# Kernel optimization log

Measured on AMD Instinct MI355X. Metric: run time of the kernel, lower is better.

Reference implementation:

```python
import jax, jax.numpy as jnp
import numpy as np

C = 4        # num_case (3) + coreference (1)
H = 128      # self.hidden_size
D = 768      # bert hidden size
B, S = 2, 384


def setup_inputs() -> dict:
    key = jax.random.key(0)
    ks = jax.random.split(key, 9)
    sc = 0.02
    return {
        "sequence_output": jax.random.normal(ks[0], (B, S, D), jnp.float32),
        "base_score": jax.random.uniform(ks[1], (B, S, C, S), jnp.float32),
        "W_prd_w": jax.random.normal(ks[2], (D, C * H), jnp.float32) * sc,
        "W_prd_b": jnp.zeros((C * H,), jnp.float32),
        "U_arg_w": jax.random.normal(ks[3], (D, C * H), jnp.float32) * sc,
        "U_arg_b": jnp.zeros((C * H,), jnp.float32),
        "W_mid": jax.random.normal(ks[4], (H * (C + 2), H), jnp.float32) * sc,
        "b_mid": jnp.zeros((H,), jnp.float32),
        "w_out": jax.random.normal(ks[5], (H,), jnp.float32) * sc,
    }


def reference(sequence_output, base_score, W_prd_w, W_prd_b, U_arg_w, U_arg_b, W_mid, b_mid, w_out):
    b, s, _ = sequence_output.shape
    # projections (dropout = identity in eval)
    h_p = (sequence_output @ W_prd_w + W_prd_b).reshape(b, s, C, H)   # [B,S,C,H]
    h_a = (sequence_output @ U_arg_w + U_arg_b).reshape(b, s, C, H)   # [B,S,C,H]
    # weighted_sum over argument positions: base_score[b,prd,case,arg]
    ref = jnp.einsum("bach,bpca->bpch", h_a, base_score).reshape(b, s, C * H)  # [B,S,C*H]
    # mid_layer(tanh(cat[prd_rep, h_a, ref])) == sum of three block matmuls,
    # since tanh is elementwise on each concatenated block.
    W1, W2, W3 = W_mid[:H], W_mid[H:2 * H], W_mid[2 * H:]
    t_prd = jnp.einsum("bpch,hk->bpck", jnp.tanh(h_p), W1)   # [B,Sp,C,H]
    t_arg = jnp.einsum("bach,hk->back", jnp.tanh(h_a), W2)   # [B,Sa,C,H]
    t_ref = jnp.tanh(ref) @ W3                                # [B,Sp,H]
    h_mid = (t_prd[:, :, None, :, :] + t_arg[:, None, :, :, :]
             + t_ref[:, :, None, None, :] + b_mid)            # [B,Sp,Sa,C,H]
    out = jnp.tanh(h_mid) @ w_out                             # [B,Sp,Sa,C]
    return out.transpose(0, 1, 3, 2)                          # [B,Sp,C,Sa]
```

## Files before the change

### kernel.cpp

```cpp
#include <hip/hip_runtime.h>
#include <hip/hip_bf16.h>


#define C2 2.885390081777927f

typedef __attribute__((ext_vector_type(8))) __bf16 bf16x8;
typedef __attribute__((ext_vector_type(8))) unsigned short ushort8;
typedef __attribute__((ext_vector_type(4))) float float4v;

__device__ __forceinline__ unsigned short f2bf(float f) {
  unsigned int u = __float_as_uint(f);
  u += 0x7fffu + ((u >> 16) & 1u);
  return (unsigned short)(u >> 16);
}

__device__ __forceinline__ float fast_tanh(float x) {
  float e = __builtin_amdgcn_exp2f(C2 * x);
  return 1.0f - 2.0f * __builtin_amdgcn_rcpf(1.0f + e);
}

__device__ __forceinline__ void gemm_core(
    const float* __restrict__ Abase, int lda,
    const float* __restrict__ Bbase, int ldb, int K,
    unsigned short* Alds, unsigned short* Blds,
    int ar, int ac, int bk, int bn,
    int wm0, int wn0, int col16, int quad, float4v acc[2][2])
{
  const float* Ap = Abase + (size_t)ar * lda + ac;
  const float* Bp = Bbase + (size_t)bk * ldb + bn;
  float4 a0 = ((const float4*)Ap)[0], a1 = ((const float4*)Ap)[1];
  float4 b0 = ((const float4*)Bp)[0], b1 = ((const float4*)Bp)[1];

  for (int k0 = 0; k0 < K; k0 += 32) {
    __syncthreads();
    {
      ushort8 o;
      o[0] = f2bf(a0.x); o[1] = f2bf(a0.y); o[2] = f2bf(a0.z); o[3] = f2bf(a0.w);
      o[4] = f2bf(a1.x); o[5] = f2bf(a1.y); o[6] = f2bf(a1.z); o[7] = f2bf(a1.w);
      *(ushort8*)&Alds[ar * 40 + ac] = o;
      float vv[8] = {b0.x, b0.y, b0.z, b0.w, b1.x, b1.y, b1.z, b1.w};
#pragma unroll
      for (int j = 0; j < 8; ++j) Blds[(bn + j) * 40 + bk] = f2bf(vv[j]);
    }
    __syncthreads();
    if (k0 + 32 < K) {
      const float4* An = (const float4*)(Ap + k0 + 32);
      const float4* Bn = (const float4*)(Bp + (size_t)(k0 + 32) * ldb);
      a0 = An[0]; a1 = An[1]; b0 = Bn[0]; b1 = Bn[1];
    }
    bf16x8 afrag[2], bfrag[2];
#pragma unroll
    for (int i = 0; i < 2; ++i)
      afrag[i] = __builtin_bit_cast(bf16x8,
          *(const ushort8*)&Alds[(wm0 + i * 16 + col16) * 40 + quad * 8]);
#pragma unroll
    for (int j = 0; j < 2; ++j)
      bfrag[j] = __builtin_bit_cast(bf16x8,
          *(const ushort8*)&Blds[(wn0 + j * 16 + col16) * 40 + quad * 8]);
#pragma unroll
    for (int i = 0; i < 2; ++i)
#pragma unroll
      for (int j = 0; j < 2; ++j)
        acc[i][j] = __builtin_amdgcn_mfma_f32_16x16x32_bf16(
            afrag[i], bfrag[j], acc[i][j], 0, 0, 0);
  }
}

__global__ __launch_bounds__(256) void g1_dual(
    const float* __restrict__ seq, const float* __restrict__ Wp,
    const float* __restrict__ Ua, const float* __restrict__ Wpb,
    const float* __restrict__ Uab, float* __restrict__ tanh_out,
    float* __restrict__ h_a, float* __restrict__ tref_clear)
{
  const int z = blockIdx.z;
  if (z == 2) {
    int idx = ((blockIdx.y * 8 + blockIdx.x) * 256 + threadIdx.x) * 4;
    *(float4*)&tref_clear[idx] = float4{0.f, 0.f, 0.f, 0.f};
    return;
  }
  __shared__ unsigned short Alds[64 * 40];
  __shared__ unsigned short Blds[64 * 40];
  const int tid = threadIdx.x;
  const int bn0 = blockIdx.x * 64, bm0 = blockIdx.y * 64;
  const int wid = tid >> 6, lane = tid & 63;
  const int wm0 = (wid >> 1) * 32, wn0 = (wid & 1) * 32;
  const int col16 = lane & 15, quad = lane >> 4;
  const float* B = z ? Ua : Wp;
  const float* bias = z ? Uab : Wpb;

  float4v acc[2][2];
#pragma unroll
  for (int i = 0; i < 2; ++i)
#pragma unroll
    for (int j = 0; j < 2; ++j) acc[i][j] = (float4v)(0.f);

  gemm_core(seq + (size_t)bm0 * 768, 768, B + bn0, 512, 768,
            Alds, Blds, tid >> 2, (tid & 3) * 8, tid >> 3, (tid & 7) * 8,
            wm0, wn0, col16, quad, acc);

  float* tout = tanh_out + (size_t)z * 393216;
#pragma unroll
  for (int j = 0; j < 2; ++j) {
    const int gcol = bn0 + wn0 + j * 16 + col16;
    const float bv = bias[gcol];
#pragma unroll
    for (int i = 0; i < 2; ++i)
#pragma unroll
      for (int r = 0; r < 4; ++r) {
        const int grow = bm0 + wm0 + i * 16 + quad * 4 + r;
        const float x = acc[i][j][r] + bv;
        const size_t cidx = (size_t)grow * 512 + gcol;
        tout[cidx] = fast_tanh(x);
        if (z == 1) h_a[cidx] = x;
      }
  }
}

__global__ __launch_bounds__(256) void fused_mid(
    const float* __restrict__ base, const float* __restrict__ h_a,
    const float* __restrict__ tanh_h, const float* __restrict__ Wmid,
    float* __restrict__ tprd_s, unsigned short* __restrict__ targ_s,
    float* __restrict__ tref_s)
{
  __shared__ unsigned short Alds[64 * 40];
  __shared__ unsigned short Blds[64 * 40];
  __shared__ unsigned short TA[64 * 72];
  __shared__ unsigned short TB[128 * 72];

  const int tid = threadIdx.x;
  const int bid = blockIdx.x;
  const int wid = tid >> 6, lane = tid & 63;
  const int wm0 = (wid >> 1) * 32, wn0 = (wid & 1) * 32;
  const int col16 = lane & 15, quad = lane >> 4;
  const int ar = tid >> 2, ac = (tid & 3) * 8;
  const int bk = tid >> 3, bn = (tid & 7) * 8;

  float4v acc[2][2];
#pragma unroll
  for (int i = 0; i < 2; ++i)
#pragma unroll
    for (int j = 0; j < 2; ++j) acc[i][j] = (float4v)(0.f);

  if (bid < 96) {
    const int z = bid / 12, rem = bid % 12;
    const int b = z >> 2, c = z & 3;
    const int y = rem >> 1, x = rem & 1;
    const float* A = base + (size_t)b * 589824 + c * 384 + (size_t)(y * 64) * 1536;
    const float* Bm = h_a + (size_t)b * 196608 + c * 128 + x * 64;
    gemm_core(A, 1536, Bm, 512, 384, Alds, Blds, ar, ac, bk, bn,
              wm0, wn0, col16, quad, acc);

#pragma unroll
    for (int j = 0; j < 2; ++j)
#pragma unroll
      for (int i = 0; i < 2; ++i)
#pragma unroll
        for (int r = 0; r < 4; ++r)
          TA[(wm0 + i * 16 + quad * 4 + r) * 72 + wn0 + j * 16 + col16] =
              f2bf(fast_tanh(acc[i][j][r]));
    {
      const float* W3p = Wmid + 32768 + (size_t)(c * 128 + x * 64) * 128;
      const int kr = tid >> 2, nb = (tid & 3) * 32;
#pragma unroll
      for (int q = 0; q < 8; ++q) {
        float4 v = *(const float4*)(W3p + (size_t)kr * 128 + nb + q * 4);
        TB[(nb + q * 4 + 0) * 72 + kr] = f2bf(v.x);
        TB[(nb + q * 4 + 1) * 72 + kr] = f2bf(v.y);
        TB[(nb + q * 4 + 2) * 72 + kr] = f2bf(v.z);
        TB[(nb + q * 4 + 3) * 72 + kr] = f2bf(v.w);
      }
    }
    __syncthreads();

    const int mh = wid & 1, nh = wid >> 1;
    float4v acc2[2][4];
#pragma unroll
    for (int i = 0; i < 2; ++i)
#pragma unroll
      for (int j = 0; j < 4; ++j) acc2[i][j] = (float4v)(0.f);
#pragma unroll
    for (int ks = 0; ks < 2; ++ks) {
      bf16x8 af[2], bf[4];
#pragma unroll
      for (int i = 0; i < 2; ++i)
        af[i] = __builtin_bit_cast(bf16x8,
            *(const ushort8*)&TA[(mh * 32 + i * 16 + col16) * 72 + ks * 32 + quad * 8]);
#pragma unroll
      for (int j = 0; j < 4; ++j)
        bf[j] = __builtin_bit_cast(bf16x8,
            *(const ushort8*)&TB[(nh * 64 + j * 16 + col16) * 72 + ks * 32 + quad * 8]);
#pragma unroll
      for (int i = 0; i < 2; ++i)
#pragma unroll
        for (int j = 0; j < 4; ++j)
          acc2[i][j] = __builtin_amdgcn_mfma_f32_16x16x32_bf16(
              af[i], bf[j], acc2[i][j], 0, 0, 0);
    }
#pragma unroll
    for (int j = 0; j < 4; ++j) {
      const int gcol = nh * 64 + j * 16 + col16;
#pragma unroll
      for (int i = 0; i < 2; ++i)
#pragma unroll
        for (int r = 0; r < 4; ++r) {
          const int grow = b * 384 + y * 64 + mh * 32 + i * 16 + quad * 4 + r;
          atomicAdd(&tref_s[(size_t)grow * 128 + gcol], C2 * acc2[i][j][r]);
        }
    }
  } else {
    const int idx = bid - 96;
    const int x = idx & 1, y = (idx >> 1) % 48, z = idx / 96;
    const float* A = tanh_h + (size_t)z * 393216 + (size_t)(y * 64) * 128;
    const float* Bm = Wmid + z * 16384 + x * 64;
    gemm_core(A, 128, Bm, 128, 128, Alds, Blds, ar, ac, bk, bn,
              wm0, wn0, col16, quad, acc);
#pragma unroll
    for (int j = 0; j < 2; ++j) {
      const int gcol = x * 64 + wn0 + j * 16 + col16;
#pragma unroll
      for (int i = 0; i < 2; ++i)
#pragma unroll
        for (int r = 0; r < 4; ++r) {
          const int grow = y * 64 + wm0 + i * 16 + quad * 4 + r;
          const float v = C2 * acc[i][j][r];
          const size_t cidx = (size_t)grow * 128 + gcol;
          if (z == 0) tprd_s[cidx] = v;
          else        targ_s[cidx] = f2bf(v);
        }
    }
  }
}

__global__ __launch_bounds__(256) void phase2(
    const float* __restrict__ tprd, const unsigned short* __restrict__ targ,
    const float* __restrict__ tref, const float* __restrict__ bmid,
    const float* __restrict__ wout, float* __restrict__ out)
{
  __shared__ float Es[8 * 128];
  __shared__ float Ws[128];
  __shared__ float Red[128 * 9];

  const int tid = threadIdx.x;
  const int a = tid & 127, kh = tid >> 7;
  const int p0 = blockIdx.x * 8, a0 = blockIdx.y * 128;
  const int b = blockIdx.z >> 2, c = blockIdx.z & 3;

  const uint4* grow = (const uint4*)((const unsigned int*)targ +
      (size_t)((b * 384 + a0 + a) * 4 + c) * 64 + kh * 32);
  uint4 G[8];
#pragma unroll
  for (int i = 0; i < 8; ++i) G[i] = grow[i];

  if (tid < 128) Ws[tid] = -2.f * wout[tid];
#pragma unroll
  for (int it = 0; it < 4; ++it) {
    int idx = it * 256 + tid;
    int p = idx >> 7, k = idx & 127;
    int row = b * 384 + p0 + p;
    Es[idx] = __builtin_amdgcn_exp2f(
        tprd[(size_t)(row * 4 + c) * 128 + k] +
        tref[(size_t)row * 128 + k] + C2 * bmid[k]);
  }
  float sw = 0.f;
  for (int k4 = 0; k4 < 32; ++k4) {
    float4 w = ((const float4*)wout)[k4];
    sw += w.x + w.y + w.z + w.w;
  }
  __syncthreads();

  float acc[8];
#pragma unroll
  for (int p = 0; p < 8; ++p) acc[p] = 0.f;

  const int kb0 = kh * 64;
#pragma unroll
  for (int j = 0; j < 8; ++j) {
    const uint4 gq = G[j];
    const float eg0 = __builtin_amdgcn_exp2f(__uint_as_float(gq.x << 16));
    const float eg1 = __builtin_amdgcn_exp2f(__uint_as_float(gq.x & 0xffff0000u));
    const float eg2 = __builtin_amdgcn_exp2f(__uint_as_float(gq.y << 16));
    const float eg3 = __builtin_amdgcn_exp2f(__uint_as_float(gq.y & 0xffff0000u));
    const float eg4 = __builtin_amdgcn_exp2f(__uint_as_float(gq.z << 16));
    const float eg5 = __builtin_amdgcn_exp2f(__uint_as_float(gq.z & 0xffff0000u));
    const float eg6 = __builtin_amdgcn_exp2f(__uint_as_float(gq.w << 16));
    const float eg7 = __builtin_amdgcn_exp2f(__uint_as_float(gq.w & 0xffff0000u));
    const int kb = kb0 + j * 8;
    const float4 wqA = *(const float4*)&Ws[kb];
    const float4 wqB = *(const float4*)&Ws[kb + 4];
#pragma unroll
    for (int p = 0; p < 8; ++p) {
      const float4 efA = *(const float4*)&Es[p * 128 + kb];
      const float4 efB = *(const float4*)&Es[p * 128 + kb + 4];
      float d0 = fmaf(efA.x, eg0, 1.f);
      float d1 = fmaf(efA.y, eg1, 1.f);
      float d2 = fmaf(efA.z, eg2, 1.f);
      float d3 = fmaf(efA.w, eg3, 1.f);
      float d01 = d0 * d1, d23 = d2 * d3;
      float n01 = fmaf(wqA.y, d0, wqA.x * d1);
      float n23 = fmaf(wqA.w, d2, wqA.z * d3);
      float num = fmaf(n01, d23, n23 * d01);
      acc[p] = fmaf(num, __builtin_amdgcn_rcpf(d01 * d23), acc[p]);
      d0 = fmaf(efB.x, eg4, 1.f);
      d1 = fmaf(efB.y, eg5, 1.f);
      d2 = fmaf(efB.z, eg6, 1.f);
      d3 = fmaf(efB.w, eg7, 1.f);
      d01 = d0 * d1; d23 = d2 * d3;
      n01 = fmaf(wqB.y, d0, wqB.x * d1);
      n23 = fmaf(wqB.w, d2, wqB.z * d3);
      num = fmaf(n01, d23, n23 * d01);
      acc[p] = fmaf(num, __builtin_amdgcn_rcpf(d01 * d23), acc[p]);
    }
  }

  if (kh) {
#pragma unroll
    for (int p = 0; p < 8; ++p) Red[a * 9 + p] = acc[p];
  }
  __syncthreads();
  if (!kh) {
    const size_t ob = (size_t)((b * 384 + p0) * 4 + c) * 384 + a0 + a;
#pragma unroll
    for (int p = 0; p < 8; ++p)
      out[ob + (size_t)p * 1536] = sw + acc[p] + Red[a * 9 + p];
  }
}

extern "C" void kernel_launch(void* const* d_in, const int* in_sizes, int n_in,
                              void* d_out, int out_size, void* d_ws, size_t ws_size,
                              hipStream_t stream) {
  (void)in_sizes; (void)n_in; (void)out_size; (void)ws_size;
  const float* seq  = (const float*)d_in[0];
  const float* base = (const float*)d_in[1];
  const float* Wp   = (const float*)d_in[2];
  const float* Wpb  = (const float*)d_in[3];
  const float* Ua   = (const float*)d_in[4];
  const float* Uab  = (const float*)d_in[5];
  const float* Wmid = (const float*)d_in[6];
  const float* bmid = (const float*)d_in[7];
  const float* wout = (const float*)d_in[8];
  float* out = (float*)d_out;

  float* ws = (float*)d_ws;
  float* tanh_h = ws;
  float* h_a    = ws + 786432;
  float* tprd_s = ws + 1179648;
  float* tref_s = ws + 1572864;
  unsigned short* targ_s = (unsigned short*)(ws + 1671168);

  g1_dual<<<dim3(8, 12, 3), dim3(256), 0, stream>>>(
      seq, Wp, Ua, Wpb, Uab, tanh_h, h_a, tref_s);
  fused_mid<<<dim3(288), dim3(256), 0, stream>>>(
      base, h_a, tanh_h, Wmid, tprd_s, targ_s, tref_s);
  phase2<<<dim3(48, 3, 8), dim3(256), 0, stream>>>(
      tprd_s, targ_s, tref_s, bmid, wout, out);
}
```

Baseline: 131.6 us.

## Stage targ tile in LDS with coalesced layout and process two predicate tiles per block

The targ intermediate is rewritten in a [b,c,s,k] layout so each phase2 block can load its 128-row tile with coalesced uint4 reads into padded shared memory. Each block now handles 16 predicate rows in two passes, reusing the exp(targ) operands across both and prefetching the next pass's tprd/tref into registers. The grid is halved. This raises LDS use and register pressure. The Es reuse between passes relies on the Red barrier.

```diff
diff --git a/kernel.cpp b/kernel.cpp
--- a/kernel.cpp
+++ b/kernel.cpp
@@ -223,9 +223,14 @@
         for (int r = 0; r < 4; ++r) {
           const int grow = y * 64 + wm0 + i * 16 + quad * 4 + r;
           const float v = C2 * acc[i][j][r];
-          const size_t cidx = (size_t)grow * 128 + gcol;
-          if (z == 0) tprd_s[cidx] = v;
-          else        targ_s[cidx] = f2bf(v);
+          if (z == 0) {
+            tprd_s[(size_t)grow * 128 + gcol] = v;
+          } else {
+            const int bb = grow / 1536;
+            const int rm = grow - bb * 1536;
+            const int cc = rm & 3, s = rm >> 2;
+            targ_s[(size_t)(((bb * 4 + cc) * 384) + s) * 128 + gcol] = f2bf(v);
+          }
         }
     }
   }
@@ -236,92 +241,128 @@
     const float* __restrict__ tref, const float* __restrict__ bmid,
     const float* __restrict__ wout, float* __restrict__ out)
 {
+  __shared__ unsigned int Gs[128 * 66];
   __shared__ float Es[8 * 128];
   __shared__ float Ws[128];
   __shared__ float Red[128 * 9];
 
   const int tid = threadIdx.x;
   const int a = tid & 127, kh = tid >> 7;
-  const int p0 = blockIdx.x * 8, a0 = blockIdx.y * 128;
+  const int p0a = blockIdx.x * 16, a0 = blockIdx.y * 128;
   const int b = blockIdx.z >> 2, c = blockIdx.z & 3;
 
-  const uint4* grow = (const uint4*)((const unsigned int*)targ +
-      (size_t)((b * 384 + a0 + a) * 4 + c) * 64 + kh * 32);
-  uint4 G[8];
-#pragma unroll
-  for (int i = 0; i < 8; ++i) G[i] = grow[i];
-
+  {
+    const uint4* src = (const uint4*)targ + ((size_t)((b * 4 + c) * 384 + a0) * 16);
+#pragma unroll
+    for (int it = 0; it < 8; ++it) {
+      const int u4 = it * 256 + tid;
+      const int r = u4 >> 4, c4 = u4 & 15;
+      uint4 v = src[u4];
+      unsigned int* dst = &Gs[r * 66 + c4 * 4];
+      *(uint2*)dst = uint2{v.x, v.y};
+      *(uint2*)(dst + 2) = uint2{v.z, v.w};
+    }
+  }
   if (tid < 128) Ws[tid] = -2.f * wout[tid];
-#pragma unroll
-  for (int it = 0; it < 4; ++it) {
-    int idx = it * 256 + tid;
-    int p = idx >> 7, k = idx & 127;
-    int row = b * 384 + p0 + p;
-    Es[idx] = __builtin_amdgcn_exp2f(
-        tprd[(size_t)(row * 4 + c) * 128 + k] +
-        tref[(size_t)row * 128 + k] + C2 * bmid[k]);
-  }
   float sw = 0.f;
   for (int k4 = 0; k4 < 32; ++k4) {
     float4 w = ((const float4*)wout)[k4];
     sw += w.x + w.y + w.z + w.w;
   }
+  float tp[4], tr[4], bm[4];
+#pragma unroll
+  for (int it = 0; it < 4; ++it) {
+    const int idx = it * 256 + tid;
+    const int p = idx >> 7, k = idx & 127;
+    const int row = b * 384 + p0a + p;
+    tp[it] = tprd[(size_t)(row * 4 + c) * 128 + k];
+    tr[it] = tref[(size_t)row * 128 + k];
+    bm[it] = C2 * bmid[k];
+  }
   __syncthreads();
 
-  float acc[8];
-#pragma unroll
-  for (int p = 0; p < 8; ++p) acc[p] = 0.f;
-
-  const int kb0 = kh * 64;
-#pragma unroll
-  for (int j = 0; j < 8; ++j) {
-    const uint4 gq = G[j];
-    const float eg0 = __builtin_amdgcn_exp2f(__uint_as_float(gq.x << 16));
-    const float eg1 = __builtin_amdgcn_exp2f(__uint_as_float(gq.x & 0xffff0000u));
-    const float eg2 = __builtin_amdgcn_exp2f(__uint_as_float(gq.y << 16));
-    const float eg3 = __builtin_amdgcn_exp2f(__uint_as_float(gq.y & 0xffff0000u));
-    const float eg4 = __builtin_amdgcn_exp2f(__uint_as_float(gq.z << 16));
-    const float eg5 = __builtin_amdgcn_exp2f(__uint_as_float(gq.z & 0xffff0000u));
-    const float eg6 = __builtin_amdgcn_exp2f(__uint_as_float(gq.w << 16));
-    const float eg7 = __builtin_amdgcn_exp2f(__uint_as_float(gq.w & 0xffff0000u));
-    const int kb = kb0 + j * 8;
-    const float4 wqA = *(const float4*)&Ws[kb];
-    const float4 wqB = *(const float4*)&Ws[kb + 4];
-#pragma unroll
-    for (int p = 0; p < 8; ++p) {
-      const float4 efA = *(const float4*)&Es[p * 128 + kb];
-      const float4 efB = *(const float4*)&Es[p * 128 + kb + 4];
-      float d0 = fmaf(efA.x, eg0, 1.f);
-      float d1 = fmaf(efA.y, eg1, 1.f);
-      float d2 = fmaf(efA.z, eg2, 1.f);
-      float d3 = fmaf(efA.w, eg3, 1.f);
-      float d01 = d0 * d1, d23 = d2 * d3;
-      float n01 = fmaf(wqA.y, d0, wqA.x * d1);
-      float n23 = fmaf(wqA.w, d2, wqA.z * d3);
-      float num = fmaf(n01, d23, n23 * d01);
-      acc[p] = fmaf(num, __builtin_amdgcn_rcpf(d01 * d23), acc[p]);
-      d0 = fmaf(efB.x, eg4, 1.f);
-      d1 = fmaf(efB.y, eg5, 1.f);
-      d2 = fmaf(efB.z, eg6, 1.f);
-      d3 = fmaf(efB.w, eg7, 1.f);
-      d01 = d0 * d1; d23 = d2 * d3;
-      n01 = fmaf(wqB.y, d0, wqB.x * d1);
-      n23 = fmaf(wqB.w, d2, wqB.z * d3);
-      num = fmaf(n01, d23, n23 * d01);
-      acc[p] = fmaf(num, __builtin_amdgcn_rcpf(d01 * d23), acc[p]);
-    }
-  }
-
-  if (kh) {
-#pragma unroll
-    for (int p = 0; p < 8; ++p) Red[a * 9 + p] = acc[p];
-  }
-  __syncthreads();
-  if (!kh) {
-    const size_t ob = (size_t)((b * 384 + p0) * 4 + c) * 384 + a0 + a;
-#pragma unroll
-    for (int p = 0; p < 8; ++p)
-      out[ob + (size_t)p * 1536] = sw + acc[p] + Red[a * 9 + p];
+  uint2 G2[16];
+  {
+    const unsigned int* g = &Gs[a * 66 + kh * 32];
+#pragma unroll
+    for (int j2 = 0; j2 < 16; ++j2) G2[j2] = *(const uint2*)(g + j2 * 2);
+  }
+
+  const size_t ob_base = (size_t)((b * 384) * 4 + c) * 384 + a0 + a;
+
+#pragma unroll
+  for (int jj = 0; jj < 2; ++jj) {
+#pragma unroll
+    for (int it = 0; it < 4; ++it)
+      Es[it * 256 + tid] = __builtin_amdgcn_exp2f(tp[it] + tr[it] + bm[it]);
+    __syncthreads();
+
+    if (jj == 0) {
+#pragma unroll
+      for (int it = 0; it < 4; ++it) {
+        const int idx = it * 256 + tid;
+        const int p = idx >> 7, k = idx & 127;
+        const int row = b * 384 + p0a + 8 + p;
+        tp[it] = tprd[(size_t)(row * 4 + c) * 128 + k];
+        tr[it] = tref[(size_t)row * 128 + k];
+      }
+    }
+
+    float acc[8];
+#pragma unroll
+    for (int p = 0; p < 8; ++p) acc[p] = 0.f;
+
+    const int kb0 = kh * 64;
+#pragma unroll
+    for (int j = 0; j < 8; ++j) {
+      const uint2 gA = G2[2 * j], gB = G2[2 * j + 1];
+      const float eg0 = __builtin_amdgcn_exp2f(__uint_as_float(gA.x << 16));
+      const float eg1 = __builtin_amdgcn_exp2f(__uint_as_float(gA.x & 0xffff0000u));
+      const float eg2 = __builtin_amdgcn_exp2f(__uint_as_float(gA.y << 16));
+      const float eg3 = __builtin_amdgcn_exp2f(__uint_as_float(gA.y & 0xffff0000u));
+      const float eg4 = __builtin_amdgcn_exp2f(__uint_as_float(gB.x << 16));
+      const float eg5 = __builtin_amdgcn_exp2f(__uint_as_float(gB.x & 0xffff0000u));
+      const float eg6 = __builtin_amdgcn_exp2f(__uint_as_float(gB.y << 16));
+      const float eg7 = __builtin_amdgcn_exp2f(__uint_as_float(gB.y & 0xffff0000u));
+      const int kb = kb0 + j * 8;
+      const float4 wqA = *(const float4*)&Ws[kb];
+      const float4 wqB = *(const float4*)&Ws[kb + 4];
+#pragma unroll
+      for (int p = 0; p < 8; ++p) {
+        const float4 efA = *(const float4*)&Es[p * 128 + kb];
+        const float4 efB = *(const float4*)&Es[p * 128 + kb + 4];
+        float d0 = fmaf(efA.x, eg0, 1.f);
+        float d1 = fmaf(efA.y, eg1, 1.f);
+        float d2 = fmaf(efA.z, eg2, 1.f);
+        float d3 = fmaf(efA.w, eg3, 1.f);
+        float d01 = d0 * d1, d23 = d2 * d3;
+        float n01 = fmaf(wqA.y, d0, wqA.x * d1);
+        float n23 = fmaf(wqA.w, d2, wqA.z * d3);
+        float num = fmaf(n01, d23, n23 * d01);
+        acc[p] = fmaf(num, __builtin_amdgcn_rcpf(d01 * d23), acc[p]);
+        d0 = fmaf(efB.x, eg4, 1.f);
+        d1 = fmaf(efB.y, eg5, 1.f);
+        d2 = fmaf(efB.z, eg6, 1.f);
+        d3 = fmaf(efB.w, eg7, 1.f);
+        d01 = d0 * d1; d23 = d2 * d3;
+        n01 = fmaf(wqB.y, d0, wqB.x * d1);
+        n23 = fmaf(wqB.w, d2, wqB.z * d3);
+        num = fmaf(n01, d23, n23 * d01);
+        acc[p] = fmaf(num, __builtin_amdgcn_rcpf(d01 * d23), acc[p]);
+      }
+    }
+
+    if (kh) {
+#pragma unroll
+      for (int p = 0; p < 8; ++p) Red[a * 9 + p] = acc[p];
+    }
+    __syncthreads();
+    if (!kh) {
+      const size_t ob = ob_base + (size_t)(p0a + jj * 8) * 1536;
+#pragma unroll
+      for (int p = 0; p < 8; ++p)
+        out[ob + (size_t)p * 1536] = sw + acc[p] + Red[a * 9 + p];
+    }
   }
 }
 
@@ -351,6 +392,6 @@
       seq, Wp, Ua, Wpb, Uab, tanh_h, h_a, tref_s);
   fused_mid<<<dim3(288), dim3(256), 0, stream>>>(
       base, h_a, tanh_h, Wmid, tprd_s, targ_s, tref_s);
-  phase2<<<dim3(48, 3, 8), dim3(256), 0, stream>>>(
+  phase2<<<dim3(24, 3, 8), dim3(256), 0, stream>>>(
       tprd_s, targ_s, tref_s, bmid, wout, out);
 }
```

New measurement: 134.8 us. 2.4% more time.

## Transpose targ to k-major layout and drop split-K reduction in phase2

Applied to the files above, without the earlier changes.

fused_mid now writes the bf16 t_arg tile through an LDS transpose into a [b,c,k-pair,s] layout, so phase2 can read coalesced 32-bit words per argument position. phase2 uses 128 threads, each covering the full K=128 for one argument, which removes the shared-memory Red buffer, the second barrier and the cross-half reduction. The trade-off is fewer threads per block, a 64-register G array that increases register pressure, and extra LDS work in fused_mid.

```diff
diff --git a/kernel.cpp b/kernel.cpp
--- a/kernel.cpp
+++ b/kernel.cpp
@@ -119,13 +119,14 @@
 __global__ __launch_bounds__(256) void fused_mid(
     const float* __restrict__ base, const float* __restrict__ h_a,
     const float* __restrict__ tanh_h, const float* __restrict__ Wmid,
-    float* __restrict__ tprd_s, unsigned short* __restrict__ targ_s,
+    float* __restrict__ tprd_s, unsigned int* __restrict__ targ_u,
     float* __restrict__ tref_s)
 {
-  __shared__ unsigned short Alds[64 * 40];
-  __shared__ unsigned short Blds[64 * 40];
-  __shared__ unsigned short TA[64 * 72];
-  __shared__ unsigned short TB[128 * 72];
+  __shared__ __align__(16) unsigned char smem[37888];
+  unsigned short* Alds = (unsigned short*)smem;
+  unsigned short* Blds = (unsigned short*)(smem + 5120);
+  unsigned short* TA   = (unsigned short*)(smem + 10240);
+  unsigned short* TB   = (unsigned short*)(smem + 19456);
 
   const int tid = threadIdx.x;
   const int bid = blockIdx.x;
@@ -214,49 +215,73 @@
     const float* Bm = Wmid + z * 16384 + x * 64;
     gemm_core(A, 128, Bm, 128, 128, Alds, Blds, ar, ac, bk, bn,
               wm0, wn0, col16, quad, acc);
-#pragma unroll
-    for (int j = 0; j < 2; ++j) {
-      const int gcol = x * 64 + wn0 + j * 16 + col16;
-#pragma unroll
-      for (int i = 0; i < 2; ++i)
-#pragma unroll
-        for (int r = 0; r < 4; ++r) {
-          const int grow = y * 64 + wm0 + i * 16 + quad * 4 + r;
-          const float v = C2 * acc[i][j][r];
-          const size_t cidx = (size_t)grow * 128 + gcol;
-          if (z == 0) tprd_s[cidx] = v;
-          else        targ_s[cidx] = f2bf(v);
-        }
-    }
-  }
-}
-
-__global__ __launch_bounds__(256) void phase2(
-    const float* __restrict__ tprd, const unsigned short* __restrict__ targ,
+    if (z == 0) {
+#pragma unroll
+      for (int j = 0; j < 2; ++j) {
+        const int gcol = x * 64 + wn0 + j * 16 + col16;
+#pragma unroll
+        for (int i = 0; i < 2; ++i)
+#pragma unroll
+          for (int r = 0; r < 4; ++r) {
+            const int grow = y * 64 + wm0 + i * 16 + quad * 4 + r;
+            tprd_s[(size_t)grow * 128 + gcol] = C2 * acc[i][j][r];
+          }
+      }
+    } else {
+      unsigned short* Tu = (unsigned short*)(smem + 10240);
+#pragma unroll
+      for (int j = 0; j < 2; ++j) {
+        const int gcol = x * 64 + wn0 + j * 16 + col16;
+        const int k2l = ((wn0 + j * 16 + col16) >> 1), half = gcol & 1;
+#pragma unroll
+        for (int i = 0; i < 2; ++i)
+#pragma unroll
+          for (int r = 0; r < 4; ++r) {
+            const int local = wm0 + i * 16 + quad * 4 + r;
+            const int cc = local & 3, sl = local >> 2;
+            Tu[(((cc * 32 + k2l) * 17) + sl) * 2 + half] =
+                f2bf(C2 * acc[i][j][r]);
+          }
+      }
+      __syncthreads();
+      const unsigned int* T = (const unsigned int*)Tu;
+      const int b = y / 24, s0 = (y % 24) * 16;
+#pragma unroll
+      for (int it = 0; it < 8; ++it) {
+        const int idx2 = it * 256 + tid;
+        const int cc = idx2 >> 9, k2l = (idx2 >> 4) & 31, sl = idx2 & 15;
+        targ_u[(size_t)((b * 4 + cc) * 64 + x * 32 + k2l) * 384 + s0 + sl] =
+            T[(cc * 32 + k2l) * 17 + sl];
+      }
+    }
+  }
+}
+
+__global__ __launch_bounds__(128) void phase2(
+    const float* __restrict__ tprd, const unsigned int* __restrict__ targ_u,
     const float* __restrict__ tref, const float* __restrict__ bmid,
     const float* __restrict__ wout, float* __restrict__ out)
 {
   __shared__ float Es[8 * 128];
   __shared__ float Ws[128];
-  __shared__ float Red[128 * 9];
 
   const int tid = threadIdx.x;
-  const int a = tid & 127, kh = tid >> 7;
   const int p0 = blockIdx.x * 8, a0 = blockIdx.y * 128;
   const int b = blockIdx.z >> 2, c = blockIdx.z & 3;
 
-  const uint4* grow = (const uint4*)((const unsigned int*)targ +
-      (size_t)((b * 384 + a0 + a) * 4 + c) * 64 + kh * 32);
-  uint4 G[8];
-#pragma unroll
-  for (int i = 0; i < 8; ++i) G[i] = grow[i];
-
-  if (tid < 128) Ws[tid] = -2.f * wout[tid];
-#pragma unroll
-  for (int it = 0; it < 4; ++it) {
-    int idx = it * 256 + tid;
-    int p = idx >> 7, k = idx & 127;
-    int row = b * 384 + p0 + p;
+  unsigned int G[64];
+  {
+    const unsigned int* gp = targ_u + (size_t)((b * 4 + c) * 64) * 384 + a0 + tid;
+#pragma unroll
+    for (int j2 = 0; j2 < 64; ++j2) G[j2] = gp[(size_t)j2 * 384];
+  }
+
+  Ws[tid] = -2.f * wout[tid];
+#pragma unroll
+  for (int it = 0; it < 8; ++it) {
+    const int idx = it * 128 + tid;
+    const int p = idx >> 7, k = idx & 127;
+    const int row = b * 384 + p0 + p;
     Es[idx] = __builtin_amdgcn_exp2f(
         tprd[(size_t)(row * 4 + c) * 128 + k] +
         tref[(size_t)row * 128 + k] + C2 * bmid[k]);
@@ -272,19 +297,19 @@
 #pragma unroll
   for (int p = 0; p < 8; ++p) acc[p] = 0.f;
 
-  const int kb0 = kh * 64;
-#pragma unroll
-  for (int j = 0; j < 8; ++j) {
-    const uint4 gq = G[j];
-    const float eg0 = __builtin_amdgcn_exp2f(__uint_as_float(gq.x << 16));
-    const float eg1 = __builtin_amdgcn_exp2f(__uint_as_float(gq.x & 0xffff0000u));
-    const float eg2 = __builtin_amdgcn_exp2f(__uint_as_float(gq.y << 16));
-    const float eg3 = __builtin_amdgcn_exp2f(__uint_as_float(gq.y & 0xffff0000u));
-    const float eg4 = __builtin_amdgcn_exp2f(__uint_as_float(gq.z << 16));
-    const float eg5 = __builtin_amdgcn_exp2f(__uint_as_float(gq.z & 0xffff0000u));
-    const float eg6 = __builtin_amdgcn_exp2f(__uint_as_float(gq.w << 16));
-    const float eg7 = __builtin_amdgcn_exp2f(__uint_as_float(gq.w & 0xffff0000u));
-    const int kb = kb0 + j * 8;
+#pragma unroll
+  for (int j = 0; j < 16; ++j) {
+    const unsigned int g0 = G[4 * j], g1 = G[4 * j + 1];
+    const unsigned int g2 = G[4 * j + 2], g3 = G[4 * j + 3];
+    const float eg0 = __builtin_amdgcn_exp2f(__uint_as_float(g0 << 16));
+    const float eg1 = __builtin_amdgcn_exp2f(__uint_as_float(g0 & 0xffff0000u));
+    const float eg2 = __builtin_amdgcn_exp2f(__uint_as_float(g1 << 16));
+    const float eg3 = __builtin_amdgcn_exp2f(__uint_as_float(g1 & 0xffff0000u));
+    const float eg4 = __builtin_amdgcn_exp2f(__uint_as_float(g2 << 16));
+    const float eg5 = __builtin_amdgcn_exp2f(__uint_as_float(g2 & 0xffff0000u));
+    const float eg6 = __builtin_amdgcn_exp2f(__uint_as_float(g3 << 16));
+    const float eg7 = __builtin_amdgcn_exp2f(__uint_as_float(g3 & 0xffff0000u));
+    const int kb = j * 8;
     const float4 wqA = *(const float4*)&Ws[kb];
     const float4 wqB = *(const float4*)&Ws[kb + 4];
 #pragma unroll
@@ -312,17 +337,10 @@
     }
   }
 
-  if (kh) {
-#pragma unroll
-    for (int p = 0; p < 8; ++p) Red[a * 9 + p] = acc[p];
-  }
-  __syncthreads();
-  if (!kh) {
-    const size_t ob = (size_t)((b * 384 + p0) * 4 + c) * 384 + a0 + a;
-#pragma unroll
-    for (int p = 0; p < 8; ++p)
-      out[ob + (size_t)p * 1536] = sw + acc[p] + Red[a * 9 + p];
-  }
+  const size_t ob = (size_t)((b * 384 + p0) * 4 + c) * 384 + a0 + tid;
+#pragma unroll
+  for (int p = 0; p < 8; ++p)
+    out[ob + (size_t)p * 1536] = sw + acc[p];
 }
 
 extern "C" void kernel_launch(void* const* d_in, const int* in_sizes, int n_in,
@@ -345,12 +363,12 @@
   float* h_a    = ws + 786432;
   float* tprd_s = ws + 1179648;
   float* tref_s = ws + 1572864;
-  unsigned short* targ_s = (unsigned short*)(ws + 1671168);
+  unsigned int* targ_u = (unsigned int*)(ws + 1671168);
 
   g1_dual<<<dim3(8, 12, 3), dim3(256), 0, stream>>>(
       seq, Wp, Ua, Wpb, Uab, tanh_h, h_a, tref_s);
   fused_mid<<<dim3(288), dim3(256), 0, stream>>>(
-      base, h_a, tanh_h, Wmid, tprd_s, targ_s, tref_s);
-  phase2<<<dim3(48, 3, 8), dim3(256), 0, stream>>>(
-      tprd_s, targ_s, tref_s, bmid, wout, out);
-}
+      base, h_a, tanh_h, Wmid, tprd_s, targ_u, tref_s);
+  phase2<<<dim3(48, 3, 8), dim3(128), 0, stream>>>(
+      tprd_s, targ_u, tref_s, bmid, wout, out);
+}
```

Measured after the change: 133.7 us. About the same (+1.5%).
